# Kernel optimization log

Measured on AMD Instinct MI355X. Metric: run time of the kernel, lower is better.

The kernel has to match this reference:

```python
import jax, jax.numpy as jnp
import numpy as np

M, B, N, D, DFF, DCOND = 8, 8, 2048, 512, 2048, 512


def setup_inputs() -> dict:
    key = jax.random.key(0)
    ks = jax.random.split(key, 8)
    s = 0.02  # weight init scale
    return {
        "x": jax.random.normal(ks[0], (B, N, D), dtype=jnp.float32),
        "cond": jax.random.normal(ks[1], (B, DCOND), dtype=jnp.float32),
        "route": jax.random.randint(ks[2], (B,), 0, M, dtype=jnp.int64),
        "W_cond": jax.random.normal(ks[3], (M, DCOND, 2 * D), dtype=jnp.float32) * s,
        "b_cond": jnp.zeros((M, 2 * D), dtype=jnp.float32),
        "W1": jax.random.normal(ks[4], (M, D, DFF), dtype=jnp.float32) * s,
        "b1": jnp.zeros((M, DFF), dtype=jnp.float32),
        "W2": jax.random.normal(ks[5], (M, DFF, D), dtype=jnp.float32) * s,
        "b2": jnp.zeros((M, D), dtype=jnp.float32),
    }


def reference(x, cond, route, W_cond, b_cond, W1, b1, W2, b2):
    # --- all branches computed densely (faithful to the torch module) ---
    # cond modulation per branch: [M, B, 2D]
    mod = jnp.einsum('bc,mcd->mbd', cond, W_cond) + b_cond[:, None, :]
    scale, shift = jnp.split(mod, 2, axis=-1)            # each [M, B, D]
    # FiLM modulate tokens: [M, B, N, D]
    x_mod = x[None] * (1.0 + scale[:, :, None, :]) + shift[:, :, None, :]
    # MLP per branch
    h = jax.nn.gelu(jnp.einsum('mbnd,mdf->mbnf', x_mod, W1) + b1[:, None, None, :])
    stacked = jnp.einsum('mbnf,mfd->mbnd', h, W2) + b2[:, None, None, :]  # [M,B,N,D]
    # --- one-hot select (torch.einsum('mbnd,bm->bnd', stacked, one_hot)) ---
    one_hot = jax.nn.one_hot(route, M, dtype=stacked.dtype)  # [B, M]
    return jnp.einsum('mbnd,bm->bnd', stacked, one_hot)
```

## Files before the change

### kernel.cpp

```cpp
#include <hip/hip_runtime.h>
#include <hip/hip_bf16.h>
#include <cstdint>
#include <cstddef>

#define NEXP   8
#define BATCH  8
#define NTOK   2048
#define DDIM   512
#define DFFDIM 2048
#define DCOND  512

typedef float  f32x4  __attribute__((ext_vector_type(4)));
typedef __bf16 bf16x8 __attribute__((ext_vector_type(8)));

using as1_cvoid = __attribute__((address_space(1))) const void;
using as3_void  = __attribute__((address_space(3))) void;

__device__ __forceinline__ void async_copy16(const void* g, void* l) {
  __builtin_amdgcn_global_load_lds((as1_cvoid*)g, (as3_void*)l, 16, 0, 0);
}

__device__ __forceinline__ unsigned short f2bf_bits(float f) {
  __hip_bfloat16 h = __float2bfloat16(f);
  return *reinterpret_cast<unsigned short*>(&h);
}

__device__ __forceinline__ float gelu_fast(float v) {
  float y = v * fmaf(0.0713548162726f, v * v, 1.5957691216057f);
  float e = exp2f(-1.44269504089f * y);
  return v * __builtin_amdgcn_rcpf(1.0f + e);
}

__global__ void mod_kernel(const float* __restrict__ cond,
                           const int* __restrict__ route,
                           const float* __restrict__ W_cond,
                           const float* __restrict__ b_cond,
                           float* __restrict__ ss) {
  const int b = blockIdx.y;
  const int m = route[b];
  const int tj = threadIdx.x & 63;
  const int cq = threadIdx.x >> 6;
  const int j = blockIdx.x * 64 + tj;
  const float* wc = W_cond + (size_t)m * DCOND * (2 * DDIM);
  const float* cb = cond + (size_t)b * DCOND;
  float acc = 0.f;
#pragma unroll 4
  for (int c = cq * 128; c < cq * 128 + 128; ++c)
    acc += cb[c] * wc[(size_t)c * (2 * DDIM) + j];
  __shared__ float red[4][64];
  red[cq][tj] = acc;
  __syncthreads();
  if (cq == 0) {
    float v = red[0][tj] + red[1][tj] + red[2][tj] + red[3][tj];
    ss[(size_t)b * (2 * DDIM) + j] = v + b_cond[(size_t)m * (2 * DDIM) + j];
  }
}

__global__ void film_kernel(const float* __restrict__ x,
                            const float* __restrict__ ss,
                            __hip_bfloat16* __restrict__ xmod) {
  const size_t idx = (size_t)blockIdx.x * blockDim.x + threadIdx.x;
  const int d4 = (int)(idx & (DDIM / 4 - 1));
  const int b  = (int)(idx >> 18);
  const float4 xv = reinterpret_cast<const float4*>(x)[idx];
  const float4 sc = reinterpret_cast<const float4*>(ss + (size_t)b * 1024)[d4];
  const float4 sh = reinterpret_cast<const float4*>(ss + (size_t)b * 1024 + DDIM)[d4];
  float r0 = xv.x * (1.f + sc.x) + sh.x;
  float r1 = xv.y * (1.f + sc.y) + sh.y;
  float r2 = xv.z * (1.f + sc.z) + sh.z;
  float r3 = xv.w * (1.f + sc.w) + sh.w;
  ushort4 ov;
  ov.x = f2bf_bits(r0); ov.y = f2bf_bits(r1);
  ov.z = f2bf_bits(r2); ov.w = f2bf_bits(r3);
  reinterpret_cast<ushort4*>(xmod)[idx] = ov;
}

__global__ void transpose_cvt(const float* __restrict__ in,
                              __hip_bfloat16* __restrict__ outp,
                              int L, int R,
                              const int* __restrict__ route) {
  const int mi = blockIdx.z;
  bool used = false;
#pragma unroll
  for (int b = 0; b < BATCH; ++b) used |= (route[b] == mi);
  if (!used) return;

  __shared__ float tile[32][33];
  const float* inm = in + (size_t)mi * L * R;
  __hip_bfloat16* outm = outp + (size_t)mi * L * R;
  const int r0 = blockIdx.x * 32, l0 = blockIdx.y * 32;
  const int tx = threadIdx.x, ty = threadIdx.y;
#pragma unroll
  for (int i = 0; i < 32; i += 8)
    tile[ty + i][tx] = inm[(size_t)(l0 + ty + i) * R + r0 + tx];
  __syncthreads();
#pragma unroll
  for (int i = 0; i < 32; i += 8)
    outm[(size_t)(r0 + ty + i) * L + l0 + tx] = __float2bfloat16(tile[tx][ty + i]);
}

template <int EPI>
__global__ __launch_bounds__(512, 1) void gemm_8ph(
    const __hip_bfloat16* __restrict__ A,
    const __hip_bfloat16* __restrict__ Btb,
    const float* __restrict__ biasbase,
    void* __restrict__ outbase,
    const int* __restrict__ route,
    int Mdim, int Ndim, int Kdim, int tilesX) {
  const int bid  = blockIdx.x;
  const int b    = bid & 7;
  const int tile = bid >> 3;
  const int bx   = tile % tilesX;
  const int by   = tile / tilesX;
  const int m = route[b];
  const __hip_bfloat16* Ab = A   + (size_t)b * Mdim * Kdim;
  const __hip_bfloat16* Bt = Btb + (size_t)m * Ndim * Kdim;
  const float* bias = biasbase + (size_t)m * Ndim;
  const int r0 = bx * 256;
  const int n0 = by * 256;

  __shared__ alignas(16) __hip_bfloat16 As[2][2][128 * 64];
  __shared__ alignas(16) __hip_bfloat16 Bs[2][2][128 * 64];

  const int t = threadIdx.x;
  const int w = t >> 6, l = t & 63;
  const int wm = w >> 2;
  const int wn = w & 3;

  const int srow = t >> 3;
  const int scol = (t & 7) ^ ((t >> 3) & 7);

#define STAGE_AH(sb, ha, k0)                                                  \
  { async_copy16(Ab + (size_t)(r0 + (ha) * 128 + srow) * Kdim + (k0) + scol * 8, \
                 &As[sb][ha][(size_t)t * 8]);                                 \
    async_copy16(Ab + (size_t)(r0 + (ha) * 128 + 64 + srow) * Kdim + (k0) + scol * 8, \
                 &As[sb][ha][(size_t)(512 + t) * 8]); }
#define STAGE_BH(sb, hb, k0)                                                  \
  { async_copy16(Bt + (size_t)(n0 + (hb) * 128 + srow) * Kdim + (k0) + scol * 8, \
                 &Bs[sb][hb][(size_t)t * 8]);                                 \
    async_copy16(Bt + (size_t)(n0 + (hb) * 128 + 64 + srow) * Kdim + (k0) + scol * 8, \
                 &Bs[sb][hb][(size_t)(512 + t) * 8]); }

  const int lrow = l & 15, lq = l >> 4, lx = l & 7;

#define LOAD_A(mh)                                                            \
  { _Pragma("unroll")                                                         \
    for (int i = 0; i < 4; ++i) {                                             \
      const int row = ((mh) * 4 + i) * 16 + lrow;                             \
      aF[i][0] = *reinterpret_cast<const bf16x8*>(&aH[(row * 8 + ((0 + lq) ^ lx)) * 8]); \
      aF[i][1] = *reinterpret_cast<const bf16x8*>(&aH[(row * 8 + ((4 + lq) ^ lx)) * 8]); \
    } }
#define LOAD_B(nh)                                                            \
  { _Pragma("unroll")                                                         \
    for (int j = 0; j < 2; ++j) {                                             \
      const int row = (wn & 1) * 64 + ((nh) * 2 + j) * 16 + lrow;             \
      bF[nh][j][0] = *reinterpret_cast<const bf16x8*>(&bH[(row * 8 + ((0 + lq) ^ lx)) * 8]); \
      bF[nh][j][1] = *reinterpret_cast<const bf16x8*>(&bH[(row * 8 + ((4 + lq) ^ lx)) * 8]); \
    } }
#define MFMA_Q(mh, nh)                                                        \
  { __builtin_amdgcn_s_setprio(1);                                            \
    _Pragma("unroll")                                                         \
    for (int i = 0; i < 4; ++i)                                               \
      _Pragma("unroll")                                                       \
      for (int j = 0; j < 2; ++j) {                                           \
        acc[(mh) * 4 + i][(nh) * 2 + j] = __builtin_amdgcn_mfma_f32_16x16x32_bf16( \
            aF[i][0], bF[nh][j][0], acc[(mh) * 4 + i][(nh) * 2 + j], 0, 0, 0);\
        acc[(mh) * 4 + i][(nh) * 2 + j] = __builtin_amdgcn_mfma_f32_16x16x32_bf16( \
            aF[i][1], bF[nh][j][1], acc[(mh) * 4 + i][(nh) * 2 + j], 0, 0, 0);\
      }                                                                       \
    __builtin_amdgcn_s_setprio(0); }
#define BARSCHED  { __builtin_amdgcn_s_barrier(); __builtin_amdgcn_sched_barrier(0); }

  f32x4 acc[8][4] = {};
  const int nt = Kdim >> 6;

  STAGE_BH(0, 0, 0)
  STAGE_AH(0, 0, 0)
  STAGE_AH(0, 1, 0)
  STAGE_BH(0, 1, 0)
  if (nt > 1) { STAGE_BH(1, 0, 64) STAGE_AH(1, 0, 64) }

  for (int kt = 0; kt < nt; ++kt) {
    const int s = kt & 1;
    if (kt == nt - 1) { asm volatile("s_waitcnt vmcnt(0)" ::: "memory"); }
    else              { asm volatile("s_waitcnt vmcnt(4)" ::: "memory"); }
    BARSCHED

    const __hip_bfloat16* aH = As[s][wm];
    const __hip_bfloat16* bH = Bs[s][wn >> 1];
    bf16x8 aF[4][2], bF[2][2][2];

    LOAD_A(0)
    LOAD_B(0)
    if (kt + 1 < nt) STAGE_AH(s ^ 1, 1, (kt + 1) * 64)
    BARSCHED
    MFMA_Q(0, 0)
    BARSCHED

    LOAD_B(1)
    if (kt + 1 < nt) STAGE_BH(s ^ 1, 1, (kt + 1) * 64)
    BARSCHED
    MFMA_Q(0, 1)
    BARSCHED

    LOAD_A(1)
    if (kt + 2 < nt) STAGE_BH(s, 0, (kt + 2) * 64)
    BARSCHED
    MFMA_Q(1, 0)
    BARSCHED

    if (kt + 2 < nt) STAGE_AH(s, 0, (kt + 2) * 64)
    MFMA_Q(1, 1)
  }
#undef STAGE_AH
#undef STAGE_BH
#undef LOAD_A
#undef LOAD_B
#undef MFMA_Q
#undef BARSCHED

  if (EPI == 0) {
    __hip_bfloat16* out = (__hip_bfloat16*)outbase + (size_t)b * Mdim * Ndim;
#pragma unroll
    for (int mb = 0; mb < 8; ++mb) {
      const int row = r0 + wm * 128 + mb * 16 + lq * 4;
#pragma unroll
      for (int nb = 0; nb < 4; ++nb) {
        const int col = n0 + wn * 64 + nb * 16 + lrow;
        const float bv = bias[col];
#pragma unroll
        for (int j = 0; j < 4; ++j) {
          float g = gelu_fast(acc[mb][nb][j] + bv);
          out[(size_t)(row + j) * Ndim + col] = __float2bfloat16(g);
        }
      }
    }
  } else {
    float* out = (float*)outbase + (size_t)b * Mdim * Ndim;
#pragma unroll
    for (int mb = 0; mb < 8; ++mb) {
      const int row = r0 + wm * 128 + mb * 16 + lq * 4;
#pragma unroll
      for (int nb = 0; nb < 4; ++nb) {
        const int col = n0 + wn * 64 + nb * 16 + lrow;
        const float bv = bias[col];
#pragma unroll
        for (int j = 0; j < 4; ++j)
          out[(size_t)(row + j) * Ndim + col] = acc[mb][nb][j] + bv;
      }
    }
  }
}

__global__ __launch_bounds__(512, 1) void gemm2_8ph(
    const __hip_bfloat16* __restrict__ A,
    const __hip_bfloat16* __restrict__ Btb,
    const float* __restrict__ biasbase,
    float* __restrict__ outb,
    const int* __restrict__ route,
    int Mdim, int Ndim, int Kdim, int tilesX) {
  const int bid  = blockIdx.x;
  const int b    = bid & 7;
  const int tile = bid >> 3;
  const int bx   = tile % tilesX;
  const int by   = tile / tilesX;
  const int m = route[b];
  const __hip_bfloat16* Ab = A   + (size_t)b * Mdim * Kdim;
  const __hip_bfloat16* Bt = Btb + (size_t)m * Ndim * Kdim;
  const float* bias = biasbase + (size_t)m * Ndim;
  const int r0 = bx * 256;
  const int n0 = by * 128;

  __shared__ alignas(16) __hip_bfloat16 As[2][2][128 * 64];
  __shared__ alignas(16) __hip_bfloat16 Bs[2][2][64 * 64];

  const int t = threadIdx.x;
  const int w = t >> 6, l = t & 63;
  const int wm = w >> 2;
  const int wn = w & 3;

  const int srow = t >> 3;
  const int scol = (t & 7) ^ ((t >> 3) & 7);

#define STAGE_AH2(sb, ha, k0)                                                 \
  { async_copy16(Ab + (size_t)(r0 + (ha) * 128 + srow) * Kdim + (k0) + scol * 8, \
                 &As[sb][ha][(size_t)t * 8]);                                 \
    async_copy16(Ab + (size_t)(r0 + (ha) * 128 + 64 + srow) * Kdim + (k0) + scol * 8, \
                 &As[sb][ha][(size_t)(512 + t) * 8]); }
#define STAGE_BH2(sb, hb, k0)                                                 \
  { async_copy16(Bt + (size_t)(n0 + (hb) * 64 + srow) * Kdim + (k0) + scol * 8, \
                 &Bs[sb][hb][(size_t)t * 8]); }

  const int lrow = l & 15, lq = l >> 4, lx = l & 7;

#define LOAD_A2(mh)                                                           \
  { _Pragma("unroll")                                                         \
    for (int i = 0; i < 4; ++i) {                                             \
      const int row = ((mh) * 4 + i) * 16 + lrow;                             \
      aF[i][0] = *reinterpret_cast<const bf16x8*>(&aH[(row * 8 + ((0 + lq) ^ lx)) * 8]); \
      aF[i][1] = *reinterpret_cast<const bf16x8*>(&aH[(row * 8 + ((4 + lq) ^ lx)) * 8]); \
    } }
#define LOAD_B2(nh)                                                           \
  { const int row = (wn & 1) * 32 + (nh) * 16 + lrow;                         \
    bF[nh][0] = *reinterpret_cast<const bf16x8*>(&bH[(row * 8 + ((0 + lq) ^ lx)) * 8]); \
    bF[nh][1] = *reinterpret_cast<const bf16x8*>(&bH[(row * 8 + ((4 + lq) ^ lx)) * 8]); }
#define MFMA_Q2(mh, nh)                                                       \
  { __builtin_amdgcn_s_setprio(1);                                            \
    _Pragma("unroll")                                                         \
    for (int i = 0; i < 4; ++i) {                                             \
      acc[(mh) * 4 + i][nh] = __builtin_amdgcn_mfma_f32_16x16x32_bf16(        \
          aF[i][0], bF[nh][0], acc[(mh) * 4 + i][nh], 0, 0, 0);               \
      acc[(mh) * 4 + i][nh] = __builtin_amdgcn_mfma_f32_16x16x32_bf16(        \
          aF[i][1], bF[nh][1], acc[(mh) * 4 + i][nh], 0, 0, 0);               \
    }                                                                         \
    __builtin_amdgcn_s_setprio(0); }
#define BARSCHED  { __builtin_amdgcn_s_barrier(); __builtin_amdgcn_sched_barrier(0); }

  f32x4 acc[8][2] = {};
  const int nt = Kdim >> 6;

  STAGE_AH2(0, 0, 0)
  STAGE_AH2(0, 1, 0)
  STAGE_BH2(0, 0, 0)
  STAGE_BH2(0, 1, 0)
  if (nt > 1) { STAGE_BH2(1, 0, 64) STAGE_AH2(1, 0, 64) }

  for (int kt = 0; kt < nt; ++kt) {
    const int s = kt & 1;
    if (kt == nt - 1) { asm volatile("s_waitcnt vmcnt(0)" ::: "memory"); }
    else              { asm volatile("s_waitcnt vmcnt(3)" ::: "memory"); }
    BARSCHED

    const __hip_bfloat16* aH = As[s][wm];
    const __hip_bfloat16* bH = Bs[s][wn >> 1];
    bf16x8 aF[4][2], bF[2][2];

    LOAD_A2(0)
    LOAD_B2(0)
    if (kt + 1 < nt) STAGE_AH2(s ^ 1, 1, (kt + 1) * 64)
    BARSCHED
    MFMA_Q2(0, 0)
    BARSCHED

    LOAD_B2(1)
    if (kt + 1 < nt) STAGE_BH2(s ^ 1, 1, (kt + 1) * 64)
    BARSCHED
    MFMA_Q2(0, 1)
    BARSCHED

    LOAD_A2(1)
    if (kt + 2 < nt) STAGE_BH2(s, 0, (kt + 2) * 64)
    BARSCHED
    MFMA_Q2(1, 0)
    BARSCHED

    if (kt + 2 < nt) STAGE_AH2(s, 0, (kt + 2) * 64)
    MFMA_Q2(1, 1)
  }
#undef STAGE_AH2
#undef STAGE_BH2
#undef LOAD_A2
#undef LOAD_B2
#undef MFMA_Q2
#undef BARSCHED

  float* out = outb + (size_t)b * Mdim * Ndim;
#pragma unroll
  for (int mb = 0; mb < 8; ++mb) {
    const int row = r0 + wm * 128 + mb * 16 + lq * 4;
#pragma unroll
    for (int nb = 0; nb < 2; ++nb) {
      const int col = n0 + wn * 32 + nb * 16 + lrow;
      const float bv = bias[col];
#pragma unroll
      for (int j = 0; j < 4; ++j)
        out[(size_t)(row + j) * Ndim + col] = acc[mb][nb][j] + bv;
    }
  }
}

extern "C" void kernel_launch(void* const* d_in, const int* in_sizes, int n_in,
                              void* d_out, int out_size, void* d_ws, size_t ws_size,
                              hipStream_t stream) {
  const float* x      = (const float*)d_in[0];
  const float* cond   = (const float*)d_in[1];
  const int*   route  = (const int*)d_in[2];
  const float* W_cond = (const float*)d_in[3];
  const float* b_cond = (const float*)d_in[4];
  const float* W1     = (const float*)d_in[5];
  const float* b1     = (const float*)d_in[6];
  const float* W2     = (const float*)d_in[7];
  const float* b2     = (const float*)d_in[8];
  float* out = (float*)d_out;

  const size_t SS_OFF   = 0;
  const size_t XMOD_OFF = 32768;
  const size_t W1T_OFF  = XMOD_OFF + (size_t)BATCH * NTOK * DDIM * 2;
  const size_t W2T_OFF  = W1T_OFF + (size_t)NEXP * DDIM * DFFDIM * 2;
  const size_t H_OFF    = W2T_OFF + (size_t)NEXP * DFFDIM * DDIM * 2;
  const size_t NEED     = H_OFF + (size_t)BATCH * NTOK * DFFDIM * 2;
  if (ws_size < NEED) return;

  char* ws = (char*)d_ws;
  float* ss            = (float*)(ws + SS_OFF);
  __hip_bfloat16* xmod = (__hip_bfloat16*)(ws + XMOD_OFF);
  __hip_bfloat16* w1t  = (__hip_bfloat16*)(ws + W1T_OFF);
  __hip_bfloat16* w2t  = (__hip_bfloat16*)(ws + W2T_OFF);
  __hip_bfloat16* h    = (__hip_bfloat16*)(ws + H_OFF);

  mod_kernel<<<dim3(2 * DDIM / 64, BATCH), 256, 0, stream>>>(cond, route, W_cond, b_cond, ss);

  {
    const size_t groups = (size_t)BATCH * NTOK * DDIM / 4;
    film_kernel<<<(unsigned)(groups / 256), 256, 0, stream>>>(x, ss, xmod);
  }

  transpose_cvt<<<dim3(DFFDIM / 32, DDIM / 32, NEXP), dim3(32, 8), 0, stream>>>(W1, w1t, DDIM, DFFDIM, route);
  transpose_cvt<<<dim3(DDIM / 32, DFFDIM / 32, NEXP), dim3(32, 8), 0, stream>>>(W2, w2t, DFFDIM, DDIM, route);

  gemm_8ph<0><<<(NTOK / 256) * (DFFDIM / 256) * BATCH, 512, 0, stream>>>(
      xmod, w1t, b1, h, route, NTOK, DFFDIM, DDIM, NTOK / 256);

  gemm2_8ph<<<(NTOK / 256) * (DDIM / 128) * BATCH, 512, 0, stream>>>(
      h, w2t, b2, out, route, NTOK, DDIM, DFFDIM, NTOK / 256);
}
```

Baseline: 137.5 us.

## Use 4-wave blocks for second GEMM and drop intra-phase barriers

The second GEMM moves from 8 waves to 4 waves per 256x128 tile. Each wave now computes a 128x64 sub-tile with a larger accumulator, and the staging loads are spread across fewer threads with adjusted vmcnt waits. Both GEMMs also drop the barrier between the LDS fragment loads and the MFMA phase in each quarter-step, cutting sync overhead. In exchange, the second GEMM has fewer waves to hide latency and uses more registers per wave.

```diff
diff --git a/kernel.cpp b/kernel.cpp
--- a/kernel.cpp
+++ b/kernel.cpp
@@ -193,19 +193,16 @@
     LOAD_A(0)
     LOAD_B(0)
     if (kt + 1 < nt) STAGE_AH(s ^ 1, 1, (kt + 1) * 64)
-    BARSCHED
     MFMA_Q(0, 0)
     BARSCHED
 
     LOAD_B(1)
     if (kt + 1 < nt) STAGE_BH(s ^ 1, 1, (kt + 1) * 64)
-    BARSCHED
     MFMA_Q(0, 1)
     BARSCHED
 
     LOAD_A(1)
     if (kt + 2 < nt) STAGE_BH(s, 0, (kt + 2) * 64)
-    BARSCHED
     MFMA_Q(1, 0)
     BARSCHED
 
@@ -252,7 +249,7 @@
   }
 }
 
-__global__ __launch_bounds__(512, 1) void gemm2_8ph(
+__global__ __launch_bounds__(256, 1) void gemm2_8ph4w(
     const __hip_bfloat16* __restrict__ A,
     const __hip_bfloat16* __restrict__ Btb,
     const float* __restrict__ biasbase,
@@ -276,20 +273,22 @@
 
   const int t = threadIdx.x;
   const int w = t >> 6, l = t & 63;
-  const int wm = w >> 2;
-  const int wn = w & 3;
+  const int wm = w >> 1;
+  const int wn = w & 1;
 
   const int srow = t >> 3;
   const int scol = (t & 7) ^ ((t >> 3) & 7);
 
 #define STAGE_AH2(sb, ha, k0)                                                 \
-  { async_copy16(Ab + (size_t)(r0 + (ha) * 128 + srow) * Kdim + (k0) + scol * 8, \
-                 &As[sb][ha][(size_t)t * 8]);                                 \
-    async_copy16(Ab + (size_t)(r0 + (ha) * 128 + 64 + srow) * Kdim + (k0) + scol * 8, \
-                 &As[sb][ha][(size_t)(512 + t) * 8]); }
+  { _Pragma("unroll")                                                         \
+    for (int i = 0; i < 4; ++i)                                               \
+      async_copy16(Ab + (size_t)(r0 + (ha) * 128 + i * 32 + srow) * Kdim + (k0) + scol * 8, \
+                   &As[sb][ha][(i * 256 + t) * 8]); }
 #define STAGE_BH2(sb, hb, k0)                                                 \
-  { async_copy16(Bt + (size_t)(n0 + (hb) * 64 + srow) * Kdim + (k0) + scol * 8, \
-                 &Bs[sb][hb][(size_t)t * 8]); }
+  { _Pragma("unroll")                                                         \
+    for (int i = 0; i < 2; ++i)                                               \
+      async_copy16(Bt + (size_t)(n0 + (hb) * 64 + i * 32 + srow) * Kdim + (k0) + scol * 8, \
+                   &Bs[sb][hb][(i * 256 + t) * 8]); }
 
   const int lrow = l & 15, lq = l >> 4, lx = l & 7;
 
@@ -301,22 +300,27 @@
       aF[i][1] = *reinterpret_cast<const bf16x8*>(&aH[(row * 8 + ((4 + lq) ^ lx)) * 8]); \
     } }
 #define LOAD_B2(nh)                                                           \
-  { const int row = (wn & 1) * 32 + (nh) * 16 + lrow;                         \
-    bF[nh][0] = *reinterpret_cast<const bf16x8*>(&bH[(row * 8 + ((0 + lq) ^ lx)) * 8]); \
-    bF[nh][1] = *reinterpret_cast<const bf16x8*>(&bH[(row * 8 + ((4 + lq) ^ lx)) * 8]); }
+  { _Pragma("unroll")                                                         \
+    for (int j = 0; j < 2; ++j) {                                             \
+      const int row = ((nh) * 2 + j) * 16 + lrow;                             \
+      bF[nh][j][0] = *reinterpret_cast<const bf16x8*>(&bH[(row * 8 + ((0 + lq) ^ lx)) * 8]); \
+      bF[nh][j][1] = *reinterpret_cast<const bf16x8*>(&bH[(row * 8 + ((4 + lq) ^ lx)) * 8]); \
+    } }
 #define MFMA_Q2(mh, nh)                                                       \
   { __builtin_amdgcn_s_setprio(1);                                            \
     _Pragma("unroll")                                                         \
-    for (int i = 0; i < 4; ++i) {                                             \
-      acc[(mh) * 4 + i][nh] = __builtin_amdgcn_mfma_f32_16x16x32_bf16(        \
-          aF[i][0], bF[nh][0], acc[(mh) * 4 + i][nh], 0, 0, 0);               \
-      acc[(mh) * 4 + i][nh] = __builtin_amdgcn_mfma_f32_16x16x32_bf16(        \
-          aF[i][1], bF[nh][1], acc[(mh) * 4 + i][nh], 0, 0, 0);               \
-    }                                                                         \
+    for (int i = 0; i < 4; ++i)                                               \
+      _Pragma("unroll")                                                       \
+      for (int j = 0; j < 2; ++j) {                                           \
+        acc[(mh) * 4 + i][(nh) * 2 + j] = __builtin_amdgcn_mfma_f32_16x16x32_bf16( \
+            aF[i][0], bF[nh][j][0], acc[(mh) * 4 + i][(nh) * 2 + j], 0, 0, 0);\
+        acc[(mh) * 4 + i][(nh) * 2 + j] = __builtin_amdgcn_mfma_f32_16x16x32_bf16( \
+            aF[i][1], bF[nh][j][1], acc[(mh) * 4 + i][(nh) * 2 + j], 0, 0, 0);\
+      }                                                                       \
     __builtin_amdgcn_s_setprio(0); }
 #define BARSCHED  { __builtin_amdgcn_s_barrier(); __builtin_amdgcn_sched_barrier(0); }
 
-  f32x4 acc[8][2] = {};
+  f32x4 acc[8][4] = {};
   const int nt = Kdim >> 6;
 
   STAGE_AH2(0, 0, 0)
@@ -328,29 +332,26 @@
   for (int kt = 0; kt < nt; ++kt) {
     const int s = kt & 1;
     if (kt == nt - 1) { asm volatile("s_waitcnt vmcnt(0)" ::: "memory"); }
-    else              { asm volatile("s_waitcnt vmcnt(3)" ::: "memory"); }
+    else              { asm volatile("s_waitcnt vmcnt(6)" ::: "memory"); }
     BARSCHED
 
     const __hip_bfloat16* aH = As[s][wm];
-    const __hip_bfloat16* bH = Bs[s][wn >> 1];
-    bf16x8 aF[4][2], bF[2][2];
+    const __hip_bfloat16* bH = Bs[s][wn];
+    bf16x8 aF[4][2], bF[2][2][2];
 
     LOAD_A2(0)
     LOAD_B2(0)
     if (kt + 1 < nt) STAGE_AH2(s ^ 1, 1, (kt + 1) * 64)
-    BARSCHED
     MFMA_Q2(0, 0)
     BARSCHED
 
     LOAD_B2(1)
     if (kt + 1 < nt) STAGE_BH2(s ^ 1, 1, (kt + 1) * 64)
-    BARSCHED
     MFMA_Q2(0, 1)
     BARSCHED
 
     LOAD_A2(1)
     if (kt + 2 < nt) STAGE_BH2(s, 0, (kt + 2) * 64)
-    BARSCHED
     MFMA_Q2(1, 0)
     BARSCHED
 
@@ -369,8 +370,8 @@
   for (int mb = 0; mb < 8; ++mb) {
     const int row = r0 + wm * 128 + mb * 16 + lq * 4;
 #pragma unroll
-    for (int nb = 0; nb < 2; ++nb) {
-      const int col = n0 + wn * 32 + nb * 16 + lrow;
+    for (int nb = 0; nb < 4; ++nb) {
+      const int col = n0 + wn * 64 + nb * 16 + lrow;
       const float bv = bias[col];
 #pragma unroll
       for (int j = 0; j < 4; ++j)
@@ -421,6 +422,6 @@
   gemm_8ph<0><<<(NTOK / 256) * (DFFDIM / 256) * BATCH, 512, 0, stream>>>(
       xmod, w1t, b1, h, route, NTOK, DFFDIM, DDIM, NTOK / 256);
 
-  gemm2_8ph<<<(NTOK / 256) * (DDIM / 128) * BATCH, 512, 0, stream>>>(
+  gemm2_8ph4w<<<(NTOK / 256) * (DDIM / 128) * BATCH, 256, 0, stream>>>(
       h, w2t, b2, out, route, NTOK, DDIM, DFFDIM, NTOK / 256);
 }
```

Result: no change. 138.7 us (+0.9%).
